# Kernel optimization log

Measured on AMD Instinct MI355X. Metric: run time of the kernel, lower is better.

## Reference

```python
import jax, jax.numpy as jnp
import numpy as np

IN_CH = 256
OUT_CH = 256
K = 3
STRIDE = 1
PAD = 1
NUM_EMB = 8


def setup_inputs() -> dict:
    key = jax.random.key(0)
    ks = jax.random.split(key, 6)
    B, H, W = 16, 64, 64
    x = jax.random.normal(ks[0], (B, IN_CH, H, W), dtype=jnp.float32)
    kernal_embed = jax.random.normal(ks[1], (NUM_EMB, IN_CH, OUT_CH, K, K), dtype=jnp.float32)
    # 1x1 conv params (stored as a dense [out,in] matrix) + bias
    cls_conv_w = jax.random.normal(ks[2], (IN_CH, IN_CH), dtype=jnp.float32) / np.sqrt(IN_CH)
    cls_conv_b = jax.random.normal(ks[3], (IN_CH,), dtype=jnp.float32) * 0.01
    cls_dense_w = jax.random.normal(ks[4], (NUM_EMB, IN_CH), dtype=jnp.float32) / np.sqrt(IN_CH)
    cls_dense_b = jax.random.normal(ks[5], (NUM_EMB,), dtype=jnp.float32) * 0.01
    return {"x": x, "kernal_embed": kernal_embed, "cls_conv_w": cls_conv_w,
            "cls_conv_b": cls_conv_b, "cls_dense_w": cls_dense_w, "cls_dense_b": cls_dense_b}


def reference(x, kernal_embed, cls_conv_w, cls_conv_b, cls_dense_w, cls_dense_b):
    B, C, H, W = x.shape
    # 1x1 conv -> global avg pool -> dense -> softmax weights over embeddings
    w = jnp.einsum('bchw,dc->bdhw', x, cls_conv_w) + cls_conv_b[None, :, None, None]
    pooled = jnp.mean(w, axis=(2, 3))                       # (B, C)
    logits = pooled @ cls_dense_w.T + cls_dense_b           # (B, E)
    mix = jax.nn.softmax(logits, axis=1)                    # (B, E)
    # Per-sample kernel synthesis: (B, in, out, k, k)
    kern = jnp.einsum('be,eiojk->biojk', mix, kernal_embed)
    # Faithful to torch .view(-1, in, k, k): raw reshape (mixes in/out axes as in original)
    kern = kern.reshape(B, OUT_CH, IN_CH, K, K)
    # Grouped conv with groups=B == per-sample conv via vmap
    def conv1(xi, wi):
        # xi: (C, H, W), wi: (out, in, k, k)
        return jax.lax.conv_general_dilated(
            xi[None], wi, window_strides=(STRIDE, STRIDE),
            padding=[(PAD, PAD), (PAD, PAD)],
            dimension_numbers=('NCHW', 'OIHW', 'NCHW'))[0]
    out = jax.vmap(conv1)(x, kern)                          # (B, out, H, W)
    return out
```

## Files before the change

kernel.cpp:

```cpp
#include <hip/hip_runtime.h>
#include <stdint.h>

#define B_  16
#define C_  256
#define H_  64
#define W_  64
#define P_  4096
#define E_  8
#define HP_ 66

typedef __bf16 bf16x8 __attribute__((ext_vector_type(8)));
typedef float  f32x4  __attribute__((ext_vector_type(4)));

__device__ __forceinline__ unsigned short f2bf(float f) {
    union { float f; unsigned int u; } v; v.f = f;
    unsigned int u = v.u;
    unsigned int r = (u + 0x7fffu + ((u >> 16) & 1u)) >> 16;
    return (unsigned short)r;
}

__device__ __forceinline__ void async_load16(const void* g, void* l) {
    __builtin_amdgcn_global_load_lds(
        (const __attribute__((address_space(1))) void*)g,
        (__attribute__((address_space(3))) void*)l, 16, 0, 0);
}

__global__ void k_xpose(const float* __restrict__ x, unsigned short* __restrict__ Xp,
                        float* __restrict__ xsum) {
    const int bid = blockIdx.x;
    const int b  = bid >> 8;
    const int h  = (bid >> 2) & 63;
    const int cg = bid & 3;
    const int c0 = cg << 6;
    const int tid = threadIdx.x;
    __shared__ float tile[64][65];
    {
        const int ci = tid >> 2, wseg = tid & 3;
        const float* src = x + ((size_t)(b * 256 + c0 + ci) << 12) + (h << 6) + wseg * 16;
        float s = 0.f;
#pragma unroll
        for (int i = 0; i < 4; ++i) {
            float4 v = *(const float4*)(src + i * 4);
            tile[ci][wseg * 16 + i * 4 + 0] = v.x;
            tile[ci][wseg * 16 + i * 4 + 1] = v.y;
            tile[ci][wseg * 16 + i * 4 + 2] = v.z;
            tile[ci][wseg * 16 + i * 4 + 3] = v.w;
            s += v.x + v.y + v.z + v.w;
        }
        s += __shfl_down(s, 1, 64);
        s += __shfl_down(s, 2, 64);
        if ((tid & 3) == 0) atomicAdd(&xsum[b * 256 + c0 + ci], s);
    }
    __syncthreads();
    {
        const int w = tid >> 2, cs = tid & 3;
        unsigned short ov[16] __attribute__((aligned(16)));
#pragma unroll
        for (int k = 0; k < 16; ++k) ov[k] = f2bf(tile[cs * 16 + k][w]);
        unsigned short* dst = Xp + ((size_t)((b * HP_ + h + 1) * HP_ + (w + 1)) << 8) + c0 + cs * 16;
        ((uint4*)dst)[0] = ((const uint4*)ov)[0];
        ((uint4*)dst)[1] = ((const uint4*)ov)[1];
    }
}

__global__ void k_mix(const float* __restrict__ xsum,
                      const float* __restrict__ cw, const float* __restrict__ cb,
                      const float* __restrict__ dw, const float* __restrict__ db,
                      float* __restrict__ mix) {
    const int b = blockIdx.x, tid = threadIdx.x;
    __shared__ float sxm[256];
    __shared__ float spool[256];
    __shared__ float sl[8];
    sxm[tid] = xsum[b * 256 + tid] * (1.0f / P_);
    __syncthreads();
    float a = cb[tid];
    for (int c = 0; c < 256; ++c) a += cw[tid * 256 + c] * sxm[c];
    spool[tid] = a;
    __syncthreads();
    if (tid < 8) {
        float l = db[tid];
        for (int d = 0; d < 256; ++d) l += dw[tid * 256 + d] * spool[d];
        sl[tid] = l;
    }
    __syncthreads();
    if (tid < 8) {
        float m = sl[0];
        for (int e = 1; e < 8; ++e) m = fmaxf(m, sl[e]);
        float den = 0.f;
        for (int e = 0; e < 8; ++e) den += __expf(sl[e] - m);
        mix[b * 8 + tid] = __expf(sl[tid] - m) / den;
    }
}

__global__ void k_mixkern(const float* __restrict__ KE, const float* __restrict__ mix,
                          unsigned short* __restrict__ Wg) {
    const int o    = blockIdx.x >> 1;
    const int half = blockIdx.x & 1;
    const int ic0  = half << 7;
    const int tid  = threadIdx.x;
    __shared__ float s[8][1152];
    __shared__ float smix[128];
    if (tid < 128) smix[tid] = mix[tid];
#pragma unroll
    for (int e = 0; e < 8; ++e) {
        const float* src = KE + (size_t)(e * 256 + o) * 2304 + ic0 * 9;
#pragma unroll
        for (int k = 0; k < 4; ++k) s[e][k * 256 + tid] = src[k * 256 + tid];
        if (tid < 128) s[e][1024 + tid] = src[1024 + tid];
    }
    __syncthreads();
    const int icl = tid & 127;
    const int b0  = (tid >> 7) << 3;
#pragma unroll
    for (int t = 0; t < 9; ++t) {
        float v[8];
#pragma unroll
        for (int e = 0; e < 8; ++e) v[e] = s[e][icl * 9 + t];
#pragma unroll
        for (int bb = 0; bb < 8; ++bb) {
            const int b = b0 + bb;
            float acc = 0.f;
#pragma unroll
            for (int e = 0; e < 8; ++e) acc += smix[b * 8 + e] * v[e];
            Wg[((size_t)(b * 256 + o) * 9 + t) * 256 + ic0 + icl] = f2bf(acc);
        }
    }
}

__global__ void k_border(unsigned short* __restrict__ Xp) {
    const int gid = blockIdx.x * 256 + threadIdx.x;
    const int pix = gid >> 5;
    const int chunk = gid & 31;
    const int b = pix / 260;
    const int j = pix - b * 260;
    int h, w;
    if (j < 66)       { h = 0;  w = j; }
    else if (j < 132) { h = 65; w = j - 66; }
    else { int jj = j - 132; h = 1 + (jj & 63); w = (jj < 64) ? 0 : 65; }
    const uint4 z = {0u, 0u, 0u, 0u};
    *(uint4*)(Xp + ((size_t)((b * HP_ + h) * HP_ + w) << 8) + chunk * 8) = z;
}

__global__ __launch_bounds__(256) void k_gemm(const unsigned short* __restrict__ Wg,
                                              const unsigned short* __restrict__ Xp,
                                              float* __restrict__ out) {
    __shared__ __align__(16) unsigned short lA[128 * 64];
    __shared__ __align__(16) unsigned short lB[128 * 64];
    const int tid = threadIdx.x;
    const int bid = blockIdx.x;
    const int xcd = bid & 7;
    const int g   = bid >> 3;
    const int b   = xcd + ((g >> 6) << 3);
    const int rem = g & 63;
    const int ot  = rem & 1;
    const int rp  = rem >> 1;
    const int o0  = ot << 7;
    const int h0  = rp << 1;

    const int wid  = tid >> 6;
    const int lane = tid & 63;
    const int wm   = wid >> 1;
    const int wn   = wid & 1;
    const int ql   = lane & 15;
    const int quad = lane >> 4;
    const int sw   = ql & 7;

    const int srow = tid >> 3;
    const int sseg = tid & 7;
    const int csrc = sseg ^ (srow & 7);

    f32x4 acc[4][4];
#pragma unroll
    for (int i = 0; i < 4; ++i)
#pragma unroll
        for (int j = 0; j < 4; ++j) acc[i][j] = (f32x4)0.0f;

    char* lAb = (char*)lA;
    char* lBb = (char*)lB;
    const size_t abase = (size_t)(b * 256 + o0 + srow) * 9 * 256 + csrc * 8;

    for (int t = 0; t < 9; ++t) {
        const int kh = t / 3;
        const int kw = t - kh * 3;
        for (int kc = 0; kc < 4; ++kc) {
#pragma unroll
            for (int j = 0; j < 4; ++j) {
                const unsigned short* ga = Wg + abase + (size_t)j * 32 * 9 * 256
                                           + (size_t)t * 256 + kc * 64;
                async_load16(ga, lAb + tid * 16 + j * 4096);
            }
#pragma unroll
            for (int j = 0; j < 4; ++j) {
                const int pix = srow + 32 * j;
                const int pr  = pix >> 6;
                const int w   = pix & 63;
                const unsigned short* gb = Xp
                    + ((size_t)((b * HP_ + h0 + pr + kh) * HP_ + (w + kw)) << 8)
                    + kc * 64 + csrc * 8;
                async_load16(gb, lBb + tid * 16 + j * 4096);
            }
            __syncthreads();
#pragma unroll
            for (int kk = 0; kk < 2; ++kk) {
                bf16x8 af[4], bv[4];
#pragma unroll
                for (int mi = 0; mi < 4; ++mi)
                    af[mi] = *(const bf16x8*)(lAb + (wm * 64 + mi * 16 + ql) * 128
                                              + ((((kk << 2) | quad) ^ sw) << 4));
#pragma unroll
                for (int ni = 0; ni < 4; ++ni)
                    bv[ni] = *(const bf16x8*)(lBb + (wn * 64 + ni * 16 + ql) * 128
                                              + ((((kk << 2) | quad) ^ sw) << 4));
#pragma unroll
                for (int mi = 0; mi < 4; ++mi)
#pragma unroll
                    for (int ni = 0; ni < 4; ++ni)
                        acc[mi][ni] = __builtin_amdgcn_mfma_f32_16x16x32_bf16(
                            af[mi], bv[ni], acc[mi][ni], 0, 0, 0);
            }
            __syncthreads();
        }
    }

    const int h = h0 + wn;
#pragma unroll
    for (int mi = 0; mi < 4; ++mi) {
        const int o = o0 + wm * 64 + mi * 16 + quad * 4;
#pragma unroll
        for (int ni = 0; ni < 4; ++ni) {
            const int w = ni * 16 + ql;
            float* po = out + ((size_t)(b * 256 + o) << 12) + (h << 6) + w;
#pragma unroll
            for (int r = 0; r < 4; ++r) po[(size_t)r << 12] = acc[mi][ni][r];
        }
    }
}

extern "C" void kernel_launch(void* const* d_in, const int* in_sizes, int n_in,
                              void* d_out, int out_size, void* d_ws, size_t ws_size,
                              hipStream_t stream) {
    const float* x  = (const float*)d_in[0];
    const float* KE = (const float*)d_in[1];
    const float* cw = (const float*)d_in[2];
    const float* cb = (const float*)d_in[3];
    const float* dw = (const float*)d_in[4];
    const float* db = (const float*)d_in[5];
    float* out = (float*)d_out;

    char* ws = (char*)d_ws;
    float* xsum           = (float*)(ws + 0);
    float* mix            = (float*)(ws + 16384);
    unsigned short* Wg    = (unsigned short*)(ws + 32768);
    unsigned short* Xp    = (unsigned short*)(ws + 32768 + 18874368);

    hipMemsetAsync(xsum, 0, B_ * C_ * sizeof(float), stream);
    k_xpose  <<<dim3(B_ * H_ * 4),    dim3(256), 0, stream>>>(x, Xp, xsum);
    k_border <<<dim3(520),            dim3(256), 0, stream>>>(Xp);
    k_mix    <<<dim3(B_),             dim3(256), 0, stream>>>(xsum, cw, cb, dw, db, mix);
    k_mixkern<<<dim3(C_ * 2),         dim3(256), 0, stream>>>(KE, mix, Wg);
    k_gemm   <<<dim3(B_ * 2 * 32),    dim3(256), 0, stream>>>(Wg, Xp, out);
}
```

Measured before the change: 267.2 us.

## Double-buffer LDS tiles to overlap async global loads with MFMA compute

Splits the shared A and B tiles into two buffers and flattens the 9x4 reduction loop into 36 stages. The async global-to-LDS loads for stage s+1 are issued before computing stage s, so memory latency can hide behind the MFMA work. This also halves the number of barriers per stage. In exchange the kernel uses twice the LDS per block, which can lower the number of resident blocks per CU.

```diff
diff --git a/kernel.cpp b/kernel.cpp
--- a/kernel.cpp
+++ b/kernel.cpp
@@ -144,8 +144,8 @@
 __global__ __launch_bounds__(256) void k_gemm(const unsigned short* __restrict__ Wg,
                                               const unsigned short* __restrict__ Xp,
                                               float* __restrict__ out) {
-    __shared__ __align__(16) unsigned short lA[128 * 64];
-    __shared__ __align__(16) unsigned short lB[128 * 64];
+    __shared__ __align__(16) unsigned short lA[2][128 * 64];
+    __shared__ __align__(16) unsigned short lB[2][128 * 64];
     const int tid = threadIdx.x;
     const int bid = blockIdx.x;
     const int xcd = bid & 7;
@@ -175,52 +175,69 @@
 #pragma unroll
         for (int j = 0; j < 4; ++j) acc[i][j] = (f32x4)0.0f;
 
-    char* lAb = (char*)lA;
-    char* lBb = (char*)lB;
     const size_t abase = (size_t)(b * 256 + o0 + srow) * 9 * 256 + csrc * 8;
 
-    for (int t = 0; t < 9; ++t) {
-        const int kh = t / 3;
-        const int kw = t - kh * 3;
-        for (int kc = 0; kc < 4; ++kc) {
-#pragma unroll
-            for (int j = 0; j < 4; ++j) {
-                const unsigned short* ga = Wg + abase + (size_t)j * 32 * 9 * 256
-                                           + (size_t)t * 256 + kc * 64;
-                async_load16(ga, lAb + tid * 16 + j * 4096);
-            }
-#pragma unroll
-            for (int j = 0; j < 4; ++j) {
-                const int pix = srow + 32 * j;
-                const int pr  = pix >> 6;
-                const int w   = pix & 63;
-                const unsigned short* gb = Xp
-                    + ((size_t)((b * HP_ + h0 + pr + kh) * HP_ + (w + kw)) << 8)
-                    + kc * 64 + csrc * 8;
-                async_load16(gb, lBb + tid * 16 + j * 4096);
-            }
-            __syncthreads();
-#pragma unroll
-            for (int kk = 0; kk < 2; ++kk) {
-                bf16x8 af[4], bv[4];
-#pragma unroll
-                for (int mi = 0; mi < 4; ++mi)
-                    af[mi] = *(const bf16x8*)(lAb + (wm * 64 + mi * 16 + ql) * 128
-                                              + ((((kk << 2) | quad) ^ sw) << 4));
-#pragma unroll
-                for (int ni = 0; ni < 4; ++ni)
-                    bv[ni] = *(const bf16x8*)(lBb + (wn * 64 + ni * 16 + ql) * 128
-                                              + ((((kk << 2) | quad) ^ sw) << 4));
-#pragma unroll
-                for (int mi = 0; mi < 4; ++mi)
-#pragma unroll
-                    for (int ni = 0; ni < 4; ++ni)
-                        acc[mi][ni] = __builtin_amdgcn_mfma_f32_16x16x32_bf16(
-                            af[mi], bv[ni], acc[mi][ni], 0, 0, 0);
-            }
-            __syncthreads();
-        }
-    }
+#define STAGE(BUF, S) do {                                                       \
+        const int s_  = (S);                                                     \
+        const int t_  = s_ >> 2;                                                 \
+        const int kc_ = s_ & 3;                                                  \
+        const int kh_ = t_ / 3;                                                  \
+        const int kw_ = t_ - kh_ * 3;                                            \
+        char* la_ = (char*)lA[BUF];                                              \
+        char* lb_ = (char*)lB[BUF];                                              \
+        _Pragma("unroll")                                                        \
+        for (int j = 0; j < 4; ++j) {                                            \
+            const unsigned short* ga = Wg + abase + (size_t)j * 32 * 9 * 256     \
+                                       + (size_t)t_ * 256 + kc_ * 64;            \
+            async_load16(ga, la_ + tid * 16 + j * 4096);                         \
+        }                                                                        \
+        _Pragma("unroll")                                                        \
+        for (int j = 0; j < 4; ++j) {                                            \
+            const int pix = srow + 32 * j;                                       \
+            const int pr  = pix >> 6;                                            \
+            const int w_  = pix & 63;                                            \
+            const unsigned short* gb = Xp                                        \
+                + ((size_t)((b * HP_ + h0 + pr + kh_) * HP_ + (w_ + kw_)) << 8)  \
+                + kc_ * 64 + csrc * 8;                                           \
+            async_load16(gb, lb_ + tid * 16 + j * 4096);                         \
+        }                                                                        \
+    } while (0)
+
+#define COMPUTE(BUF) do {                                                        \
+        char* la_ = (char*)lA[BUF];                                              \
+        char* lb_ = (char*)lB[BUF];                                              \
+        _Pragma("unroll")                                                        \
+        for (int kk = 0; kk < 2; ++kk) {                                         \
+            bf16x8 af[4], bv[4];                                                 \
+            _Pragma("unroll")                                                    \
+            for (int mi = 0; mi < 4; ++mi)                                       \
+                af[mi] = *(const bf16x8*)(la_ + (wm * 64 + mi * 16 + ql) * 128   \
+                                          + ((((kk << 2) | quad) ^ sw) << 4));   \
+            _Pragma("unroll")                                                    \
+            for (int ni = 0; ni < 4; ++ni)                                       \
+                bv[ni] = *(const bf16x8*)(lb_ + (wn * 64 + ni * 16 + ql) * 128   \
+                                          + ((((kk << 2) | quad) ^ sw) << 4));   \
+            _Pragma("unroll")                                                    \
+            for (int mi = 0; mi < 4; ++mi)                                       \
+                _Pragma("unroll")                                                \
+                for (int ni = 0; ni < 4; ++ni)                                   \
+                    acc[mi][ni] = __builtin_amdgcn_mfma_f32_16x16x32_bf16(       \
+                        af[mi], bv[ni], acc[mi][ni], 0, 0, 0);                   \
+        }                                                                        \
+    } while (0)
+
+    STAGE(0, 0);
+    __syncthreads();
+    for (int s = 0; s < 36; s += 2) {
+        STAGE(1, s + 1);
+        COMPUTE(0);
+        __syncthreads();
+        if (s + 2 < 36) STAGE(0, s + 2);
+        COMPUTE(1);
+        __syncthreads();
+    }
+#undef STAGE
+#undef COMPUTE
 
     const int h = h0 + wn;
 #pragma unroll
```

New measurement: 273.0 us. 1.02x slower.
